# Optimization experiments

Measured on AMD Instinct MI355X. Metric: run time of the kernel, lower is better.

The kernel has to match this reference:

```python
import jax, jax.numpy as jnp
import numpy as np

EPS = 1e-5

def _layernorm(x, gamma, beta):
    mu = jnp.mean(x, axis=-1, keepdims=True)
    var = jnp.var(x, axis=-1, keepdims=True)
    return (x - mu) * jax.lax.rsqrt(var + EPS) * gamma + beta

def setup_inputs() -> dict:
    key = jax.random.key(0)
    ks = jax.random.split(key, 6)
    bs, t, dim = 4, 2048, 1024
    x = jax.random.normal(ks[0], (bs, t, dim), dtype=jnp.float32)
    # shared LayerNorm params (same module applied twice in forward)
    ln_gamma = jnp.ones((dim,), dtype=jnp.float32)
    ln_beta = jnp.zeros((dim,), dtype=jnp.float32)
    # Linear params, stored as (in, out)
    w1 = jax.random.normal(ks[1], (dim, 2 * dim), dtype=jnp.float32) / np.sqrt(dim)
    b1 = jax.random.normal(ks[2], (2 * dim,), dtype=jnp.float32) * 0.01
    w2 = jax.random.normal(ks[3], (2 * dim, dim), dtype=jnp.float32) / np.sqrt(2 * dim)
    b2 = jax.random.normal(ks[4], (dim,), dtype=jnp.float32) * 0.01
    return {"x": x, "ln_gamma": ln_gamma, "ln_beta": ln_beta,
            "w1": w1, "b1": b1, "w2": w2, "b2": b2}

def reference(x, ln_gamma, ln_beta, w1, b1, w2, b2):
    # x: [bs, t, f]
    y = _layernorm(x, ln_gamma, ln_beta)
    y = jax.nn.gelu(jnp.einsum('btf,fh->bth', y, w1) + b1, approximate=False)
    y = jnp.einsum('bth,hf->btf', y, w2) + b2
    # attention-like quadratic mix (no softmax): (x @ x^T) @ y
    scores = jnp.einsum('btf,bsf->bts', x, x)          # [bs, t, t]
    y = jnp.einsum('bts,bsf->btf', scores, y)
    y = x + y
    y = _layernorm(y, ln_gamma, ln_beta)
    return y
```

## Files before the change

kernel.cpp:

```cpp
#include <hip/hip_runtime.h>
#include <hip/hip_fp16.h>

typedef _Float16 f16;
typedef _Float16 f16x8 __attribute__((ext_vector_type(8)));
typedef _Float16 f16x4 __attribute__((ext_vector_type(4)));
typedef float f32x4 __attribute__((ext_vector_type(4)));

#define LN_EPS 1e-5f

__device__ __forceinline__ float erf_fast(float x) {
    const float ax = __builtin_fabsf(x);
    const float t = 1.0f / (1.0f + 0.3275911f * ax);
    const float y = t * (0.254829592f +
                    t * (-0.284496736f +
                    t * (1.421413741f +
                    t * (-1.453152027f +
                    t * 1.061405429f))));
    const float r = 1.0f - y * __expf(-ax * ax);
    return __builtin_copysignf(r, x);
}

__device__ __forceinline__ float gelu_exact(float v) {
    return 0.5f * v * (1.0f + erf_fast(v * 0.70710678118654752440f));
}

__device__ __forceinline__ void gload_lds16(const f16* g, f16* l) {
    __builtin_amdgcn_global_load_lds(
        (const __attribute__((address_space(1))) unsigned int*)(g),
        (__attribute__((address_space(3))) unsigned int*)(l),
        16, 0, 0);
}

__global__ __launch_bounds__(256)
void ln_cast_kernel(const float* __restrict__ x,
                    const float* __restrict__ gamma,
                    const float* __restrict__ beta,
                    f16* __restrict__ y_h,
                    f16* __restrict__ x_h) {
    const int row = blockIdx.x;
    const int t = threadIdx.x;
    const size_t base = (size_t)row * 1024;
    float4 v = ((const float4*)(x + base))[t];
    float s  = v.x + v.y + v.z + v.w;
    float s2 = v.x*v.x + v.y*v.y + v.z*v.z + v.w*v.w;
    #pragma unroll
    for (int off = 32; off > 0; off >>= 1) {
        s  += __shfl_down(s, off, 64);
        s2 += __shfl_down(s2, off, 64);
    }
    __shared__ float ls[4], ls2[4];
    const int wid = t >> 6;
    if ((t & 63) == 0) { ls[wid] = s; ls2[wid] = s2; }
    __syncthreads();
    if (t == 0) {
        ls[0]  = ls[0] + ls[1] + ls[2] + ls[3];
        ls2[0] = ls2[0] + ls2[1] + ls2[2] + ls2[3];
    }
    __syncthreads();
    const float mu   = ls[0] * (1.0f / 1024.0f);
    const float var  = ls2[0] * (1.0f / 1024.0f) - mu * mu;
    const float rstd = rsqrtf(var + LN_EPS);
    const float4 g  = ((const float4*)gamma)[t];
    const float4 bt = ((const float4*)beta)[t];
    f16x4 yo, xo;
    yo[0] = (f16)((v.x - mu) * rstd * g.x + bt.x);
    yo[1] = (f16)((v.y - mu) * rstd * g.y + bt.y);
    yo[2] = (f16)((v.z - mu) * rstd * g.z + bt.z);
    yo[3] = (f16)((v.w - mu) * rstd * g.w + bt.w);
    xo[0] = (f16)v.x; xo[1] = (f16)v.y; xo[2] = (f16)v.z; xo[3] = (f16)v.w;
    *(f16x4*)(y_h + base + t * 4) = yo;
    *(f16x4*)(x_h + base + t * 4) = xo;
}

__global__ __launch_bounds__(256)
void ln_final_kernel(const float* __restrict__ pre,
                     const float* __restrict__ gamma,
                     const float* __restrict__ beta,
                     float* __restrict__ out) {
    const int row = blockIdx.x;
    const int t = threadIdx.x;
    const size_t base = (size_t)row * 1024;
    float4 v = ((const float4*)(pre + base))[t];
    float s  = v.x + v.y + v.z + v.w;
    float s2 = v.x*v.x + v.y*v.y + v.z*v.z + v.w*v.w;
    #pragma unroll
    for (int off = 32; off > 0; off >>= 1) {
        s  += __shfl_down(s, off, 64);
        s2 += __shfl_down(s2, off, 64);
    }
    __shared__ float ls[4], ls2[4];
    const int wid = t >> 6;
    if ((t & 63) == 0) { ls[wid] = s; ls2[wid] = s2; }
    __syncthreads();
    if (t == 0) {
        ls[0]  = ls[0] + ls[1] + ls[2] + ls[3];
        ls2[0] = ls2[0] + ls2[1] + ls2[2] + ls2[3];
    }
    __syncthreads();
    const float mu   = ls[0] * (1.0f / 1024.0f);
    const float var  = ls2[0] * (1.0f / 1024.0f) - mu * mu;
    const float rstd = rsqrtf(var + LN_EPS);
    const float4 g  = ((const float4*)gamma)[t];
    const float4 bt = ((const float4*)beta)[t];
    float4 o;
    o.x = (v.x - mu) * rstd * g.x + bt.x;
    o.y = (v.y - mu) * rstd * g.y + bt.y;
    o.z = (v.z - mu) * rstd * g.z + bt.z;
    o.w = (v.w - mu) * rstd * g.w + bt.w;
    ((float4*)(out + base))[t] = o;
}

__global__ __launch_bounds__(256)
void transpose_cast_kernel(const float* __restrict__ src,
                           f16* __restrict__ dst, int R, int C) {
    __shared__ float tile[32][33];
    const int c0 = blockIdx.x * 32, r0 = blockIdx.y * 32;
    const int tx = threadIdx.x & 31, ty = threadIdx.x >> 5;
    #pragma unroll
    for (int i = 0; i < 4; ++i) {
        const int r = ty + i * 8;
        tile[r][tx] = src[(size_t)(r0 + r) * C + c0 + tx];
    }
    __syncthreads();
    #pragma unroll
    for (int i = 0; i < 4; ++i) {
        const int r = ty + i * 8;
        dst[(size_t)(c0 + r) * R + r0 + tx] = (f16)tile[tx][r];
    }
}

__global__ __launch_bounds__(256)
void transpose_f16_kernel(const f16* __restrict__ src,
                          f16* __restrict__ dst, int R, int C) {
    __shared__ f16 tile[32][33];
    const size_t zb = (size_t)blockIdx.z * R * C;
    src += zb; dst += zb;
    const int c0 = blockIdx.x * 32, r0 = blockIdx.y * 32;
    const int tx = threadIdx.x & 31, ty = threadIdx.x >> 5;
    #pragma unroll
    for (int i = 0; i < 4; ++i) {
        const int r = ty + i * 8;
        tile[r][tx] = src[(size_t)(r0 + r) * C + c0 + tx];
    }
    __syncthreads();
    #pragma unroll
    for (int i = 0; i < 4; ++i) {
        const int r = ty + i * 8;
        dst[(size_t)(c0 + r) * R + r0 + tx] = tile[tx][r];
    }
}

template <int EPI>
__global__ __launch_bounds__(512, 2)
void gemm256x128_nt_kernel(const f16* __restrict__ A, const f16* __restrict__ Bt,
                           const float* __restrict__ bias,
                           const float* __restrict__ xadd,
                           f16* __restrict__ outH, float* __restrict__ outF,
                           int M, int N, int K,
                           long long batchA, long long batchB, long long batchC) {
    __shared__ __attribute__((aligned(16))) f16 sA[3][256 * 64];
    __shared__ __attribute__((aligned(16))) f16 sB[3][128 * 64];

    const int z = blockIdx.z;
    A  += (size_t)z * batchA;
    Bt += (size_t)z * batchB;

    const int m0 = blockIdx.x * 256;
    const int n0 = blockIdx.y * 128;
    const int t = threadIdx.x;
    const int l = t & 63;
    const int wid = t >> 6;
    const int wr = wid >> 1;
    const int wc = wid & 1;
    const int rl = l & 15;
    const int g  = l >> 4;
    const int nk = K >> 6;

    const int rowS = t >> 3;
    const int kbS  = ((t & 7) ^ (rowS & 7)) * 8;
    const f16* pA = A  + (size_t)(m0 + rowS) * K + kbS;
    const f16* pB = Bt + (size_t)(n0 + rowS) * K + kbS;
    const int ldsS = wid * 512;

    const int rA = wr * 64 + rl;
    const int rB = wc * 64 + rl;
    const int swk0 = ((g)     ^ (rl & 7)) * 8;
    const int swk1 = ((4 + g) ^ (rl & 7)) * 8;

    f32x4 acc[4][4] = {};

    auto mf = [&](f32x4 c, f16x8 af, f16x8 bf) {
        if constexpr (EPI != 1)
            return __builtin_amdgcn_mfma_f32_16x16x32_f16(bf, af, c, 0, 0, 0);
        else
            return __builtin_amdgcn_mfma_f32_16x16x32_f16(af, bf, c, 0, 0, 0);
    };

    auto stgA = [&](f16* dst, int u, int kc) {
        gload_lds16(pA + (size_t)u * 64 * K + kc * 64, dst + u * 4096 + ldsS);
    };
    auto stgB = [&](f16* dst, int u, int kc) {
        gload_lds16(pB + (size_t)u * 64 * K + kc * 64, dst + u * 4096 + ldsS);
    };

    const int t1 = (nk > 1) ? 1 : 0;
    #pragma unroll
    for (int u = 0; u < 4; ++u) stgA(sA[0], u, 0);
    #pragma unroll
    for (int u = 0; u < 2; ++u) stgB(sB[0], u, 0);
    #pragma unroll
    for (int u = 0; u < 4; ++u) stgA(sA[1], u, t1);
    #pragma unroll
    for (int u = 0; u < 2; ++u) stgB(sB[1], u, t1);

    f16 *curA = sA[0], *nxtA = sA[1], *farA = sA[2];
    f16 *curB = sB[0], *nxtB = sB[1], *farB = sB[2];

    f16x8 a[4][2], b[4][2];

    for (int kt = 0; kt < nk; ++kt) {
        asm volatile("s_waitcnt vmcnt(6)" ::: "memory");
        __builtin_amdgcn_s_barrier();
        asm volatile("" ::: "memory");

        const int kt2 = (kt + 2 < nk) ? kt + 2 : nk - 1;

        #pragma unroll
        for (int fm = 0; fm < 4; ++fm) {
            a[fm][0] = *(const f16x8*)(curA + (rA + fm * 16) * 64 + swk0);
            a[fm][1] = *(const f16x8*)(curA + (rA + fm * 16) * 64 + swk1);
        }
        #pragma unroll
        for (int fn = 0; fn < 4; ++fn) {
            b[fn][0] = *(const f16x8*)(curB + (rB + fn * 16) * 64 + swk0);
            b[fn][1] = *(const f16x8*)(curB + (rB + fn * 16) * 64 + swk1);
        }
        stgA(farA, 0, kt2);
        stgA(farA, 1, kt2);
        stgA(farA, 2, kt2);
        stgA(farA, 3, kt2);
        stgB(farB, 0, kt2);
        stgB(farB, 1, kt2);

        #pragma unroll
        for (int fm = 0; fm < 4; ++fm)
            #pragma unroll
            for (int fn = 0; fn < 4; ++fn) {
                acc[fm][fn] = mf(acc[fm][fn], a[fm][0], b[fn][0]);
                acc[fm][fn] = mf(acc[fm][fn], a[fm][1], b[fn][1]);
            }

        f16* tp;
        tp = curA; curA = nxtA; nxtA = farA; farA = tp;
        tp = curB; curB = nxtB; nxtB = farB; farB = tp;
    }
    asm volatile("s_waitcnt vmcnt(0)" ::: "memory");

    if (EPI == 1) {
        #pragma unroll
        for (int fm = 0; fm < 4; ++fm) {
            #pragma unroll
            for (int fn = 0; fn < 4; ++fn) {
                const int col = n0 + wc * 64 + fn * 16 + rl;
                const int row0 = m0 + wr * 64 + fm * 16 + g * 4;
                const int zz = row0 >> 11;
                const int rr = row0 & 2047;
                const float bv = bias[col];
                f16x4 o;
                #pragma unroll
                for (int r = 0; r < 4; ++r) o[r] = (f16)(acc[fm][fn][r] + bv);
                *(f16x4*)(outH + ((size_t)zz * N + col) * 2048 + rr) = o;
            }
        }
    } else {
        const float* xaddz = xadd;
        float* outFz = outF;
        if (EPI == 3) {
            outFz += (size_t)z * batchC;
            xaddz += (size_t)z * batchC;
        }
        #pragma unroll
        for (int fm = 0; fm < 4; ++fm) {
            const int row = m0 + wr * 64 + fm * 16 + rl;
            #pragma unroll
            for (int fn = 0; fn < 4; ++fn) {
                const int colb = n0 + wc * 64 + fn * 16 + g * 4;
                if (EPI == 0) {
                    const float4 bv = *(const float4*)&bias[colb];
                    f16x4 o;
                    o[0] = (f16)gelu_exact(acc[fm][fn][0] + bv.x);
                    o[1] = (f16)gelu_exact(acc[fm][fn][1] + bv.y);
                    o[2] = (f16)gelu_exact(acc[fm][fn][2] + bv.z);
                    o[3] = (f16)gelu_exact(acc[fm][fn][3] + bv.w);
                    *(f16x4*)(outH + (size_t)row * N + colb) = o;
                } else {
                    const size_t idx = (size_t)row * N + colb;
                    const float4 xa = *(const float4*)&xaddz[idx];
                    float4 o;
                    o.x = acc[fm][fn][0] + xa.x;
                    o.y = acc[fm][fn][1] + xa.y;
                    o.z = acc[fm][fn][2] + xa.z;
                    o.w = acc[fm][fn][3] + xa.w;
                    *(float4*)(outFz + idx) = o;
                }
            }
        }
    }
}

__global__ __launch_bounds__(256, 3)
void gemm_nt_kernel(const f16* __restrict__ A, const f16* __restrict__ Bt,
                    f16* __restrict__ outH,
                    int M, int N, int K,
                    long long batchA, long long batchB, long long batchC) {
    __shared__ __attribute__((aligned(16))) f16 sA[3][128 * 32];
    __shared__ __attribute__((aligned(16))) f16 sB[3][128 * 32];

    const int z = blockIdx.z;
    A  += (size_t)z * batchA;
    Bt += (size_t)z * batchB;

    const int m0 = blockIdx.x * 128;
    const int n0 = blockIdx.y * 128;
    const int t = threadIdx.x;
    const int l = t & 63;
    const int wid = t >> 6;
    const int wm = (wid >> 1) * 64;
    const int wn = (wid & 1) * 64;

    f32x4 acc[4][4] = {};

    const int rl = l & 15;
    const int nk = K >> 5;

    const int row0 = t >> 2;
    const int kb = ((t & 3) ^ (row0 & 3)) * 8;
    const f16* Ag0 = A  + (size_t)(m0 + row0) * K + kb;
    const f16* Ag1 = A  + (size_t)(m0 + row0 + 64) * K + kb;
    const f16* Bg0 = Bt + (size_t)(n0 + row0) * K + kb;
    const f16* Bg1 = Bt + (size_t)(n0 + row0 + 64) * K + kb;
    const int lo0 = wid * 512;
    const int lo1 = 2048 + wid * 512;

    const int swk = (((l >> 4) ^ (rl & 3))) * 8;

    gload_lds16(Ag0,      sA[0] + lo0);
    gload_lds16(Ag1,      sA[0] + lo1);
    gload_lds16(Bg0,      sB[0] + lo0);
    gload_lds16(Bg1,      sB[0] + lo1);
    gload_lds16(Ag0 + 32, sA[1] + lo0);
    gload_lds16(Ag1 + 32, sA[1] + lo1);
    gload_lds16(Bg0 + 32, sB[1] + lo0);
    gload_lds16(Bg1 + 32, sB[1] + lo1);

    f16 *curA = sA[0], *nxtA = sA[1], *farA = sA[2];
    f16 *curB = sB[0], *nxtB = sB[1], *farB = sB[2];

    for (int kt = 0; kt < nk; ++kt) {
        asm volatile("s_waitcnt vmcnt(4)" ::: "memory");
        __builtin_amdgcn_s_barrier();
        asm volatile("" ::: "memory");

        const int ktn = (kt + 2 < nk) ? kt + 2 : nk - 1;
        const int kof = ktn * 32;
        gload_lds16(Ag0 + kof, farA + lo0);
        gload_lds16(Ag1 + kof, farA + lo1);
        gload_lds16(Bg0 + kof, farB + lo0);
        gload_lds16(Bg1 + kof, farB + lo1);

        f16x8 a[4], b[4];
        #pragma unroll
        for (int f = 0; f < 4; ++f) {
            a[f] = *(const f16x8*)&curA[(wm + f * 16 + rl) * 32 + swk];
            b[f] = *(const f16x8*)&curB[(wn + f * 16 + rl) * 32 + swk];
        }
        #pragma unroll
        for (int fm = 0; fm < 4; ++fm)
            #pragma unroll
            for (int fn = 0; fn < 4; ++fn)
                acc[fm][fn] = __builtin_amdgcn_mfma_f32_16x16x32_f16(
                    b[fn], a[fm], acc[fm][fn], 0, 0, 0);

        f16* tA = curA; curA = nxtA; nxtA = farA; farA = tA;
        f16* tB = curB; curB = nxtB; nxtB = farB; farB = tB;
    }
    asm volatile("s_waitcnt vmcnt(0)" ::: "memory");

    const int rh = l >> 4;
    f16* outHz = outH + (size_t)z * batchC;
    #pragma unroll
    for (int fm = 0; fm < 4; ++fm) {
        const int row = m0 + wm + fm * 16 + rl;
        #pragma unroll
        for (int fn = 0; fn < 4; ++fn) {
            const int colb = n0 + wn + fn * 16 + rh * 4;
            f16x4 o;
            #pragma unroll
            for (int r = 0; r < 4; ++r) o[r] = (f16)acc[fm][fn][r];
            *(f16x4*)(outHz + (size_t)row * N + colb) = o;
        }
    }
}

extern "C" void kernel_launch(void* const* d_in, const int* in_sizes, int n_in,
                              void* d_out, int out_size, void* d_ws, size_t ws_size,
                              hipStream_t stream) {
    const float* x     = (const float*)d_in[0];
    const float* gamma = (const float*)d_in[1];
    const float* beta  = (const float*)d_in[2];
    const float* w1    = (const float*)d_in[3];
    const float* b1    = (const float*)d_in[4];
    const float* w2    = (const float*)d_in[5];
    const float* b2    = (const float*)d_in[6];
    float* out = (float*)d_out;

    const int BS = 4, T = 2048, DIM = 1024, HID = 2048;
    const int M = BS * T;
    const long long MB = 1024 * 1024;

    char* ws = (char*)d_ws;
    f16*   x_h  = (f16*)(ws + 0 * MB);
    f16*   y_h  = (f16*)(ws + 16 * MB);
    f16*   h    = (f16*)(ws + 32 * MB);
    float* pre  = (float*)h;
    f16*   y2t  = (f16*)(ws + 64 * MB);
    f16*   x_t  = (f16*)(ws + 80 * MB);
    f16*   G    = (f16*)(ws + 96 * MB);
    f16*   w1t  = (f16*)(ws + 104 * MB);
    f16*   w2t  = (f16*)(ws + 108 * MB);

    ln_cast_kernel<<<M, 256, 0, stream>>>(x, gamma, beta, y_h, x_h);

    transpose_cast_kernel<<<dim3(HID / 32, DIM / 32), 256, 0, stream>>>(w1, w1t, DIM, HID);
    transpose_cast_kernel<<<dim3(DIM / 32, HID / 32), 256, 0, stream>>>(w2, w2t, HID, DIM);

    gemm256x128_nt_kernel<0><<<dim3(M / 256, HID / 128, 1), 512, 0, stream>>>(
        y_h, w1t, b1, nullptr, h, nullptr, M, HID, DIM, 0, 0, 0);

    gemm256x128_nt_kernel<1><<<dim3(M / 256, DIM / 128, 1), 512, 0, stream>>>(
        h, w2t, b2, nullptr, y2t, nullptr, M, DIM, HID, 0, 0, 0);

    transpose_f16_kernel<<<dim3(DIM / 32, T / 32, BS), 256, 0, stream>>>(x_h, x_t, T, DIM);

    gemm_nt_kernel<<<dim3(DIM / 128, DIM / 128, BS), 256, 0, stream>>>(
        y2t, x_t, G, DIM, DIM, T,
        (long long)DIM * T, (long long)DIM * T, (long long)DIM * DIM);

    gemm256x128_nt_kernel<3><<<dim3(T / 256, DIM / 128, BS), 512, 0, stream>>>(
        x_h, G, nullptr, x, nullptr, pre, T, DIM, DIM,
        (long long)T * DIM, (long long)DIM * DIM, (long long)T * DIM);

    ln_final_kernel<<<M, 256, 0, stream>>>(pre, gamma, beta, out);
}
```

Before: 204.6 us.

## Halve GEMM K-tile to 32 to fit four blocks per CU

Shrinks the per-stage K depth of the 256x128 GEMM from 64 to 32. This halves the triple-buffered LDS footprint and the fragment registers, and launch bounds are raised to allow 4 blocks per CU for more latency hiding. The swizzle, staging addressing and wait counts are adjusted to match, and the global-to-LDS prefetch is now issued before the LDS fragment reads. In exchange there are twice as many iterations, each with a barrier and less MFMA work, and register pressure may force spills under the tighter bound.

```diff
diff --git a/kernel.cpp b/kernel.cpp
--- a/kernel.cpp
+++ b/kernel.cpp
@@ -151,15 +151,15 @@
 }
 
 template <int EPI>
-__global__ __launch_bounds__(512, 2)
+__global__ __launch_bounds__(512, 4)
 void gemm256x128_nt_kernel(const f16* __restrict__ A, const f16* __restrict__ Bt,
                            const float* __restrict__ bias,
                            const float* __restrict__ xadd,
                            f16* __restrict__ outH, float* __restrict__ outF,
                            int M, int N, int K,
                            long long batchA, long long batchB, long long batchC) {
-    __shared__ __attribute__((aligned(16))) f16 sA[3][256 * 64];
-    __shared__ __attribute__((aligned(16))) f16 sB[3][128 * 64];
+    __shared__ __attribute__((aligned(16))) f16 sA[3][256 * 32];
+    __shared__ __attribute__((aligned(16))) f16 sB[3][128 * 32];
 
     const int z = blockIdx.z;
     A  += (size_t)z * batchA;
@@ -174,18 +174,17 @@
     const int wc = wid & 1;
     const int rl = l & 15;
     const int g  = l >> 4;
-    const int nk = K >> 6;
-
-    const int rowS = t >> 3;
-    const int kbS  = ((t & 7) ^ (rowS & 7)) * 8;
+    const int nk = K >> 5;
+
+    const int rowS = t >> 2;
+    const int kbS  = ((t & 3) ^ (rowS & 3)) * 8;
     const f16* pA = A  + (size_t)(m0 + rowS) * K + kbS;
     const f16* pB = Bt + (size_t)(n0 + rowS) * K + kbS;
     const int ldsS = wid * 512;
 
     const int rA = wr * 64 + rl;
     const int rB = wc * 64 + rl;
-    const int swk0 = ((g)     ^ (rl & 7)) * 8;
-    const int swk1 = ((4 + g) ^ (rl & 7)) * 8;
+    const int swk = (g ^ (rl & 3)) * 8;
 
     f32x4 acc[4][4] = {};
 
@@ -197,58 +196,44 @@
     };
 
     auto stgA = [&](f16* dst, int u, int kc) {
-        gload_lds16(pA + (size_t)u * 64 * K + kc * 64, dst + u * 4096 + ldsS);
+        gload_lds16(pA + (size_t)u * 128 * K + kc * 32, dst + u * 4096 + ldsS);
     };
-    auto stgB = [&](f16* dst, int u, int kc) {
-        gload_lds16(pB + (size_t)u * 64 * K + kc * 64, dst + u * 4096 + ldsS);
+    auto stgB = [&](f16* dst, int kc) {
+        gload_lds16(pB + kc * 32, dst + ldsS);
     };
 
     const int t1 = (nk > 1) ? 1 : 0;
-    #pragma unroll
-    for (int u = 0; u < 4; ++u) stgA(sA[0], u, 0);
-    #pragma unroll
-    for (int u = 0; u < 2; ++u) stgB(sB[0], u, 0);
-    #pragma unroll
-    for (int u = 0; u < 4; ++u) stgA(sA[1], u, t1);
-    #pragma unroll
-    for (int u = 0; u < 2; ++u) stgB(sB[1], u, t1);
+    stgA(sA[0], 0, 0); stgA(sA[0], 1, 0); stgB(sB[0], 0);
+    stgA(sA[1], 0, t1); stgA(sA[1], 1, t1); stgB(sB[1], t1);
 
     f16 *curA = sA[0], *nxtA = sA[1], *farA = sA[2];
     f16 *curB = sB[0], *nxtB = sB[1], *farB = sB[2];
 
-    f16x8 a[4][2], b[4][2];
+    f16x8 a[4], b[4];
 
     for (int kt = 0; kt < nk; ++kt) {
-        asm volatile("s_waitcnt vmcnt(6)" ::: "memory");
+        asm volatile("s_waitcnt vmcnt(3)" ::: "memory");
         __builtin_amdgcn_s_barrier();
         asm volatile("" ::: "memory");
 
         const int kt2 = (kt + 2 < nk) ? kt + 2 : nk - 1;
 
-        #pragma unroll
-        for (int fm = 0; fm < 4; ++fm) {
-            a[fm][0] = *(const f16x8*)(curA + (rA + fm * 16) * 64 + swk0);
-            a[fm][1] = *(const f16x8*)(curA + (rA + fm * 16) * 64 + swk1);
-        }
-        #pragma unroll
-        for (int fn = 0; fn < 4; ++fn) {
-            b[fn][0] = *(const f16x8*)(curB + (rB + fn * 16) * 64 + swk0);
-            b[fn][1] = *(const f16x8*)(curB + (rB + fn * 16) * 64 + swk1);
-        }
         stgA(farA, 0, kt2);
         stgA(farA, 1, kt2);
-        stgA(farA, 2, kt2);
-        stgA(farA, 3, kt2);
-        stgB(farB, 0, kt2);
-        stgB(farB, 1, kt2);
+        stgB(farB, kt2);
+
+        #pragma unroll
+        for (int fm = 0; fm < 4; ++fm)
+            a[fm] = *(const f16x8*)(curA + (rA + fm * 16) * 32 + swk);
+        #pragma unroll
+        for (int fn = 0; fn < 4; ++fn)
+            b[fn] = *(const f16x8*)(curB + (rB + fn * 16) * 32 + swk);
 
         #pragma unroll
         for (int fm = 0; fm < 4; ++fm)
             #pragma unroll
-            for (int fn = 0; fn < 4; ++fn) {
-                acc[fm][fn] = mf(acc[fm][fn], a[fm][0], b[fn][0]);
-                acc[fm][fn] = mf(acc[fm][fn], a[fm][1], b[fn][1]);
-            }
+            for (int fn = 0; fn < 4; ++fn)
+                acc[fm][fn] = mf(acc[fm][fn], a[fm], b[fn]);
 
         f16* tp;
         tp = curA; curA = nxtA; nxtA = farA; farA = tp;
```

Result: slower. 231.8 us (+13.3%).
